# Performance work log

Hardware: AMD Instinct MI355X
Metric: run time of the kernel (lower is better)

The kernel has to match this reference:

```python
import jax, jax.numpy as jnp
import numpy as np

# Hodgkin-Huxley / synaptic constants (CFG in the original repo)
GNA, GK, GL = 40.0, 35.0, 0.1
ENA, EK, EL = 55.0, -77.0, -65.0
GS, VS = 0.5, 0.0
IAPP = 0.5
VT, KP = -20.0, 3.0
A_D, A_R = 1.0, 0.1
DT = 0.05


def setup_inputs() -> dict:
    key = jax.random.key(0)
    B, N, L = 32, 2000, 128
    z = jax.random.uniform(key, (B, N, L), dtype=jnp.float32)
    return {"z": z}


def _hh_step(carry, z_prev):
    V, m, n, h, y = carry  # each (B, L)
    pow1 = GNA * m ** 3 * h
    pow2 = GK * n ** 4
    G = DT / 2 * (pow1 + pow2 + GL + GS * y)
    E = pow1 * ENA + pow2 * EK + GL * EL + GS * VS * y
    Vn = (V * (1 - G) + DT * (E + IAPP)) / (1 + G)

    aN = 0.02 * (Vn - 25) / (1 - jnp.exp((-Vn + 25) / 9.0))
    aM = 0.182 * (Vn + 35) / (1 - jnp.exp((-Vn - 35) / 9.0))
    aH = 0.25 * jnp.exp((-Vn - 90) / 12.0)
    bN = -0.002 * (Vn - 25) / (1 - jnp.exp((Vn - 25) / 9.0))
    bM = -0.124 * (Vn + 35) / (1 - jnp.exp((Vn + 35) / 9.0))
    bH = 0.25 * jnp.exp((Vn + 34) / 12.0)
    # removable-singularity fixups (exact equality, as in the original)
    at25 = Vn == 25.0
    atm35 = Vn == -35.0
    aN = jnp.where(at25, 0.18, aN)
    bN = jnp.where(at25, 0.08, bN)
    aM = jnp.where(atm35, 1.638, aM)
    bM = jnp.where(atm35, 1.16, bM)

    def cn(a, b, x):  # semi-implicit (Crank-Nicolson) gating update
        s = DT / 2 * (a + b)
        return (a * DT + (1 - s) * x) / (s + 1)

    mn = cn(aM, bM, m)
    nn = cn(aN, bN, n)
    hn = cn(aH, bH, h)
    sy = DT / 2 * (A_D * z_prev + A_R)
    yn = (A_D * z_prev * DT + (1 - sy) * y) / (sy + 1)
    return (Vn, mn, nn, hn, yn), Vn


def reference(z):
    B, N, L = z.shape
    V0 = jnp.full((B, L), -70.0, dtype=z.dtype)
    m0 = jnp.zeros((B, L), dtype=z.dtype)
    n0 = jnp.zeros((B, L), dtype=z.dtype)
    h0 = jnp.ones((B, L), dtype=z.dtype)
    y0 = jnp.zeros((B, L), dtype=z.dtype)
    zs = jnp.moveaxis(z[:, :-1, :], 1, 0)  # (N-1, B, L)
    _, V_seq = jax.lax.scan(_hh_step, (V0, m0, n0, h0, y0), zs)
    V_all = jnp.concatenate([V0[None], V_seq], axis=0)  # (N, B, L)
    V_all = jnp.moveaxis(V_all, 0, 1)  # (B, N, L)
    return jax.nn.sigmoid((V_all - VT) / KP)
```

## Files before the change

kernel.cpp:

```cpp
#include <hip/hip_runtime.h>


#if defined(__HIP_DEVICE_COMPILE__)
#define EXP2 __builtin_amdgcn_exp2f
#else
#define EXP2 exp2f
#endif

__device__ __forceinline__ float rcpf(float x) { return __builtin_amdgcn_rcpf(x); }

template<int CTRL>
__device__ __forceinline__ float qp(float x) {
#if defined(__HIP_DEVICE_COMPILE__)
    return __int_as_float(__builtin_amdgcn_mov_dpp(__float_as_int(x), CTRL, 0xF, 0xF, false));
#else
    return x;
#endif
}
#define QB0(x) qp<0x00>(x)
#define QB1(x) qp<0x55>(x)
#define QB2(x) qp<0xAA>(x)
#define QB3(x) qp<0xFF>(x)
#define QSW(x) qp<0xB1>(x)

struct LaneC {
    float cA, cB, cC, cD, cE, cW, cV, cZ, cH, cX, cY, sing, fixA, fixS;
};

__device__ __forceinline__ float hh_step4(float& V, float& g, float z,
                                          const LaneC& C, bool is23) {
    float nn = QB0(g), mm = QB1(g), hh = QB2(g), yy = QB3(g);
    float m2 = mm * mm, mh = mm * hh;
    float p1 = m2 * mh;
    float q  = nn * nn, n4 = q * q;
    float gy = __builtin_fmaf(0.0125f, yy, 0.0025f);
    float pg = p1 + gy;
    float G  = __builtin_fmaf(0.875f, n4, pg);
    float rd = rcpf(G + 1.0f);
    float t1 = __builtin_fmaf(110.0f, p1, V - 0.3f);
    float t2 = __builtin_fmaf(-134.75f, n4, t1);
    float Vn = __builtin_fmaf(-V, G, t2) * rd;
    float E  = EXP2(__builtin_fmaf(C.cA, Vn, C.cB));
    float t  = __builtin_fmaf(C.cC, Vn, C.cD);
    float u  = rcpf(__builtin_fmaf(-C.cE, E, 1.0f));
    float w  = C.cW * E;
    float a  = __builtin_fmaf(t, u, __builtin_fmaf(C.cV, w, C.cZ * z));
    float br = QSW(w);
    float b  = __builtin_fmaf(C.cX, br, C.cY);
    float s1 = a * __builtin_fmaf(C.cH, E, 0.025f);
    float s2 = 0.025f * (a + b);
    float s  = is23 ? s2 : s1;
    bool fx  = (Vn == C.sing);
    a = fx ? C.fixA : a;
    s = fx ? C.fixS : s;
    float r  = rcpf(s + 1.0f);
    g = __builtin_fmaf(0.05f, a, __builtin_fmaf(-s, g, g)) * r;
    V = Vn;
    return Vn;
}

__global__ __launch_bounds__(64, 1)
void hh_kernel(const float* __restrict__ z, float* __restrict__ out, int N) {
    const int gid   = blockIdx.x * 64 + threadIdx.x;
    const int lane  = gid & 3;
    const int chain = gid >> 2;
    const int b = chain >> 7;
    const int l = chain & 127;
    const size_t base = (size_t)b * N * 128 + l;
    const float* zp = z + base;
    float* op = out + base;
    const bool is0  = (lane == 0);
    const bool is23 = (lane & 2) != 0;

    LaneC C;
    const float NaNf = __int_as_float(0x7FC00000);
    switch (lane) {
    case 0:
        C = { -0.1602994490f,  4.0074862250f, 0.02f, -0.5f, 1.0f, 0.0f, 0.0f, 0.0f,
              0.0025f, 0.0f, 0.0f, 25.0f, 0.18f, 0.0065f };
        break;
    case 1:
        C = { -0.1602994490f, -5.6104807150f, 0.182f, 6.37f, 1.0f, 0.0f, 0.0f, 0.0f,
              0.0170329670329670f, 0.0f, 0.0f, -35.0f, 1.638f, 0.06995f };
        break;
    case 2:
        C = { -0.1202245839f, -10.8202125510f, 0.0f, 0.0f, 0.0f, 0.25f, 1.0f, 0.0f,
              0.0f, 1.0f, 0.0f, NaNf, 0.0f, 0.0f };
        break;
    default:
        C = {  0.1202245839f,   4.0876358530f, 0.0f, 0.0f, 0.0f, 0.25f, 0.0f, 1.0f,
              0.0f, 0.0f, 0.1f, NaNf, 0.0f, 0.0f };
        break;
    }

    float V = -70.0f;
    float g = (lane == 2) ? 1.0f : 0.0f;

    if (is0) op[0] = -70.0f;

    float z0 = (0 <= N-2) ? zp[0]     : 0.0f;
    float z1 = (1 <= N-2) ? zp[128]   : 0.0f;
    float z2 = (2 <= N-2) ? zp[256]   : 0.0f;
    float z3 = (3 <= N-2) ? zp[384]   : 0.0f;
    float z4 = (4 <= N-2) ? zp[512]   : 0.0f;
    float z5 = (5 <= N-2) ? zp[640]   : 0.0f;
    float z6 = (6 <= N-2) ? zp[768]   : 0.0f;
    float z7 = (7 <= N-2) ? zp[896]   : 0.0f;
    const float* zpre = zp + 8 * 128;
    float* o = op + 128;
    int t = 1;
    for (; t <= N - 11; t += 4) {
        float q0 = zpre[0];
        float q1 = zpre[128];
        float q2 = zpre[256];
        float q3 = zpre[384];
        zpre += 512;
        float v0 = hh_step4(V, g, z0, C, is23);
        float v1 = hh_step4(V, g, z1, C, is23);
        float v2 = hh_step4(V, g, z2, C, is23);
        float v3 = hh_step4(V, g, z3, C, is23);
        if (is0) { o[0] = v0; o[128] = v1; o[256] = v2; o[384] = v3; }
        o += 512;
        z0 = z4; z1 = z5; z2 = z6; z3 = z7;
        z4 = q0; z5 = q1; z6 = q2; z7 = q3;
    }
    for (; t < N; ++t) {
        float v0 = hh_step4(V, g, z0, C, is23);
        if (is0) *o = v0;
        o += 128;
        z0 = z1; z1 = z2; z2 = z3; z3 = z4; z4 = z5; z5 = z6; z6 = z7;
        z7 = (t + 7 <= N - 1) ? zpre[0] : 0.0f;
        zpre += 128;
    }
}

__global__ __launch_bounds__(256)
void sig_kernel(float4* __restrict__ v, int n4c) {
    int i = blockIdx.x * 256 + threadIdx.x;
    if (i < n4c) {
        float4 x = v[i];
        x.x = rcpf(1.0f + EXP2(__builtin_fmaf(-0.48089834664f, x.x, -9.6179669328f)));
        x.y = rcpf(1.0f + EXP2(__builtin_fmaf(-0.48089834664f, x.y, -9.6179669328f)));
        x.z = rcpf(1.0f + EXP2(__builtin_fmaf(-0.48089834664f, x.z, -9.6179669328f)));
        x.w = rcpf(1.0f + EXP2(__builtin_fmaf(-0.48089834664f, x.w, -9.6179669328f)));
        v[i] = x;
    }
}

extern "C" void kernel_launch(void* const* d_in, const int* in_sizes, int n_in,
                              void* d_out, int out_size, void* d_ws, size_t ws_size,
                              hipStream_t stream) {
    const float* z = (const float*)d_in[0];
    float* out = (float*)d_out;
    const int B = 32, L = 128;
    const int N = in_sizes[0] / (B * L);
    dim3 grid(B * L * 4 / 64), block(64);
    hipLaunchKernelGGL(hh_kernel, grid, block, 0, stream, z, out, N);
    const int n4c = out_size / 4;
    dim3 sgrid((n4c + 255) / 256), sblock(256);
    hipLaunchKernelGGL(sig_kernel, sgrid, sblock, 0, stream, (float4*)out, n4c);
}
```

Baseline: 245.6 us.

## Reformulate gating update to shorten dependency chain and deepen z prefetch

Rewrites the per-lane Crank-Nicolson gating update as g = (beta*g + alpha)/Q, with lane-specific constants. This removes the separate reciprocal of the exp denominator and the is23 select, leaving a single reciprocal on the serial critical path. The z prefetch depth also grows from 8 to 12 steps to hide more load latency. The risks are floating-point differences from the reassociated formula and higher register pressure from the extra prefetch registers.

```diff
diff --git a/kernel.cpp b/kernel.cpp
--- a/kernel.cpp
+++ b/kernel.cpp
@@ -24,13 +24,18 @@
 #define QSW(x) qp<0xB1>(x)
 
 struct LaneC {
-    float cA, cB, cC, cD, cE, cW, cV, cZ, cH, cX, cY, sing, fixA, fixS;
+    float cA, cB;
+    float cC, cD;
+    float cE;
+    float cH, cK, cL, cM;
+    float cAe, cAz, cAt;
+    float sing, fixB, fixA, fixQ;
 };
 
 __device__ __forceinline__ float hh_step4(float& V, float& g, float z,
-                                          const LaneC& C, bool is23) {
-    float nn = QB0(g), mm = QB1(g), hh = QB2(g), yy = QB3(g);
-    float m2 = mm * mm, mh = mm * hh;
+                                          const LaneC& C) {
+    float nn = QB0(g), mm = QB1(g), hh2 = QB2(g), yy = QB3(g);
+    float m2 = mm * mm, mh = mm * hh2;
     float p1 = m2 * mh;
     float q  = nn * nn, n4 = q * q;
     float gy = __builtin_fmaf(0.0125f, yy, 0.0025f);
@@ -40,21 +45,21 @@
     float t1 = __builtin_fmaf(110.0f, p1, V - 0.3f);
     float t2 = __builtin_fmaf(-134.75f, n4, t1);
     float Vn = __builtin_fmaf(-V, G, t2) * rd;
-    float E  = EXP2(__builtin_fmaf(C.cA, Vn, C.cB));
+    float e  = EXP2(__builtin_fmaf(C.cA, Vn, C.cB));
     float t  = __builtin_fmaf(C.cC, Vn, C.cD);
-    float u  = rcpf(__builtin_fmaf(-C.cE, E, 1.0f));
-    float w  = C.cW * E;
-    float a  = __builtin_fmaf(t, u, __builtin_fmaf(C.cV, w, C.cZ * z));
-    float br = QSW(w);
-    float b  = __builtin_fmaf(C.cX, br, C.cY);
-    float s1 = a * __builtin_fmaf(C.cH, E, 0.025f);
-    float s2 = 0.025f * (a + b);
-    float s  = is23 ? s2 : s1;
     bool fx  = (Vn == C.sing);
-    a = fx ? C.fixA : a;
-    s = fx ? C.fixS : s;
-    float r  = rcpf(s + 1.0f);
-    g = __builtin_fmaf(0.05f, a, __builtin_fmaf(-s, g, g)) * r;
+    float br = QSW(e);
+    float w  = t * __builtin_fmaf(C.cH, e, C.cK);
+    float s  = __builtin_fmaf(C.cL, br, __builtin_fmaf(C.cM, z, w));
+    float u  = __builtin_fmaf(-C.cE, e, 1.0f);
+    float Q  = u + s;
+    float be = u - s;
+    float al = __builtin_fmaf(C.cAe, e, __builtin_fmaf(C.cAz, z, C.cAt * t));
+    float P  = __builtin_fmaf(be, g, al);
+    float Pf = __builtin_fmaf(C.fixB, g, C.fixA);
+    P = fx ? Pf : P;
+    Q = fx ? C.fixQ : Q;
+    g = P * rcpf(Q);
     V = Vn;
     return Vn;
 }
@@ -69,27 +74,34 @@
     const size_t base = (size_t)b * N * 128 + l;
     const float* zp = z + base;
     float* op = out + base;
-    const bool is0  = (lane == 0);
-    const bool is23 = (lane & 2) != 0;
+    const bool is0 = (lane == 0);
 
     LaneC C;
     const float NaNf = __int_as_float(0x7FC00000);
     switch (lane) {
     case 0:
-        C = { -0.1602994490f,  4.0074862250f, 0.02f, -0.5f, 1.0f, 0.0f, 0.0f, 0.0f,
-              0.0025f, 0.0f, 0.0f, 25.0f, 0.18f, 0.0065f };
+        C = { -0.1602994490f,  4.0074862250f,  0.02f, -0.5f, 1.0f,
+              0.0025f, 0.025f, 0.0f, 0.0f,
+              0.0f, 0.0f, 0.05f,
+              25.0f, 0.9935f, 0.009f, 1.0065f };
         break;
     case 1:
-        C = { -0.1602994490f, -5.6104807150f, 0.182f, 6.37f, 1.0f, 0.0f, 0.0f, 0.0f,
-              0.0170329670329670f, 0.0f, 0.0f, -35.0f, 1.638f, 0.06995f };
+        C = { -0.1602994490f, -5.6104807150f,  0.182f, 6.37f, 1.0f,
+              0.0170329670329670f, 0.025f, 0.0f, 0.0f,
+              0.0f, 0.0f, 0.05f,
+              -35.0f, 0.93005f, 0.0819f, 1.06995f };
         break;
     case 2:
-        C = { -0.1202245839f, -10.8202125510f, 0.0f, 0.0f, 0.0f, 0.25f, 1.0f, 0.0f,
-              0.0f, 1.0f, 0.0f, NaNf, 0.0f, 0.0f };
+        C = { -0.1202245839f, -10.8202125510f, 0.0f, 1.0f, 0.0f,
+              0.00625f, 0.0f, 0.00625f, 0.0f,
+              0.0125f, 0.0f, 0.0f,
+              NaNf, 0.0f, 0.0f, 1.0f };
         break;
     default:
-        C = {  0.1202245839f,   4.0876358530f, 0.0f, 0.0f, 0.0f, 0.25f, 0.0f, 1.0f,
-              0.0f, 0.0f, 0.1f, NaNf, 0.0f, 0.0f };
+        C = {  0.1202245839f,   4.0876358530f, 0.0f, 1.0f, 0.0f,
+              0.0f, 0.0025f, 0.0f, 0.025f,
+              0.0f, 0.05f, 0.0f,
+              NaNf, 0.0f, 0.0f, 1.0f };
         break;
     }
 
@@ -98,38 +110,44 @@
 
     if (is0) op[0] = -70.0f;
 
-    float z0 = (0 <= N-2) ? zp[0]     : 0.0f;
-    float z1 = (1 <= N-2) ? zp[128]   : 0.0f;
-    float z2 = (2 <= N-2) ? zp[256]   : 0.0f;
-    float z3 = (3 <= N-2) ? zp[384]   : 0.0f;
-    float z4 = (4 <= N-2) ? zp[512]   : 0.0f;
-    float z5 = (5 <= N-2) ? zp[640]   : 0.0f;
-    float z6 = (6 <= N-2) ? zp[768]   : 0.0f;
-    float z7 = (7 <= N-2) ? zp[896]   : 0.0f;
-    const float* zpre = zp + 8 * 128;
+    float zb0  = (0  <= N-2) ? zp[0]    : 0.0f;
+    float zb1  = (1  <= N-2) ? zp[128]  : 0.0f;
+    float zb2  = (2  <= N-2) ? zp[256]  : 0.0f;
+    float zb3  = (3  <= N-2) ? zp[384]  : 0.0f;
+    float zb4  = (4  <= N-2) ? zp[512]  : 0.0f;
+    float zb5  = (5  <= N-2) ? zp[640]  : 0.0f;
+    float zb6  = (6  <= N-2) ? zp[768]  : 0.0f;
+    float zb7  = (7  <= N-2) ? zp[896]  : 0.0f;
+    float zb8  = (8  <= N-2) ? zp[1024] : 0.0f;
+    float zb9  = (9  <= N-2) ? zp[1152] : 0.0f;
+    float zb10 = (10 <= N-2) ? zp[1280] : 0.0f;
+    float zb11 = (11 <= N-2) ? zp[1408] : 0.0f;
+    const float* zpre = zp + 12 * 128;
     float* o = op + 128;
     int t = 1;
-    for (; t <= N - 11; t += 4) {
+    for (; t <= N - 15; t += 4) {
         float q0 = zpre[0];
         float q1 = zpre[128];
         float q2 = zpre[256];
         float q3 = zpre[384];
         zpre += 512;
-        float v0 = hh_step4(V, g, z0, C, is23);
-        float v1 = hh_step4(V, g, z1, C, is23);
-        float v2 = hh_step4(V, g, z2, C, is23);
-        float v3 = hh_step4(V, g, z3, C, is23);
+        float v0 = hh_step4(V, g, zb0, C);
+        float v1 = hh_step4(V, g, zb1, C);
+        float v2 = hh_step4(V, g, zb2, C);
+        float v3 = hh_step4(V, g, zb3, C);
         if (is0) { o[0] = v0; o[128] = v1; o[256] = v2; o[384] = v3; }
         o += 512;
-        z0 = z4; z1 = z5; z2 = z6; z3 = z7;
-        z4 = q0; z5 = q1; z6 = q2; z7 = q3;
+        zb0 = zb4;  zb1 = zb5;  zb2 = zb6;  zb3 = zb7;
+        zb4 = zb8;  zb5 = zb9;  zb6 = zb10; zb7 = zb11;
+        zb8 = q0;   zb9 = q1;   zb10 = q2;  zb11 = q3;
     }
     for (; t < N; ++t) {
-        float v0 = hh_step4(V, g, z0, C, is23);
+        float v0 = hh_step4(V, g, zb0, C);
         if (is0) *o = v0;
         o += 128;
-        z0 = z1; z1 = z2; z2 = z3; z3 = z4; z4 = z5; z5 = z6; z6 = z7;
-        z7 = (t + 7 <= N - 1) ? zpre[0] : 0.0f;
+        zb0 = zb1; zb1 = zb2; zb2 = zb3; zb3 = zb4; zb4 = zb5; zb5 = zb6;
+        zb6 = zb7; zb7 = zb8; zb8 = zb9; zb9 = zb10; zb10 = zb11;
+        zb11 = (t + 11 <= N - 1) ? zpre[0] : 0.0f;
         zpre += 128;
     }
 }
```

New measurement: 284.8 us. 1.16x slower.
